# Optimization experiments

Measured on AMD Instinct MI355X. Metric: run time of the kernel, lower is better.

Reference implementation:

```python
import jax, jax.numpy as jnp
import numpy as np

F_BINS, T_STEPS, N_ACTIONS = 257, 65536, 256  # STFT bins, frames, codebook size


def setup_inputs() -> dict:
    key = jax.random.key(0)
    k1, k2, k3, k4 = jax.random.split(key, 4)
    x_out = jax.random.normal(k1, (F_BINS, T_STEPS), dtype=jnp.float32)
    x_source = jax.random.normal(k2, (F_BINS, T_STEPS), dtype=jnp.float32)
    x_clean = jax.random.normal(k3, (F_BINS, T_STEPS), dtype=jnp.float32)
    # G is self.G_mat = G_mat.T, i.e. [freq, action]; gains in [0,1)
    G = jax.random.uniform(k4, (F_BINS, N_ACTIONS), dtype=jnp.float32)
    return {"x_out": x_out, "x_source": x_source, "x_clean": x_clean, "G": G}


def reference(x_out, x_source, x_clean, G):
    # sums[t, a] = sum_f (x_clean[f, t] - G[f, a] * x_source[f, t])
    #            = sum_f x_clean[:, t]  -  (x_source^T @ G)[t, a]
    clean_sum = jnp.sum(x_clean, axis=0)                 # [T]
    proj = jnp.einsum('ft,fa->ta', x_source, G)          # [T, A]
    sums = clean_sum[:, None] - proj                     # [T, A]
    A_t = jnp.argmin(sums, axis=1)                       # [T], values in [0, A)
    F, T = x_source.shape
    # Faithful to the original loop: wiener_true[:, a] = G[:, a] for each
    # SELECTED ACTION a (column indexed by action id, not timestep).
    # Duplicate indices write identical values, so scatter-set is well-defined.
    wiener_true = jnp.zeros((F, T), dtype=x_source.dtype).at[:, A_t].set(G[:, A_t])
    true_out = (wiener_true * x_source).T                # [T, F]
    loss = jnp.mean((true_out - x_out.T) ** 2)
    return loss
```

## Files before the change

kernel.cpp:

```cpp
#include <hip/hip_runtime.h>

#define F_BINS  257
#define T_STEPS 65536
#define N_ACT   256
#define TM      256
#define NBLK_G  256
#define NTHR    512
#define XO_N4   4210688
#define XO_BLKS 514
#define PREP_BLKS 36

typedef float f32x4 __attribute__((ext_vector_type(4)));
typedef short s16x8 __attribute__((ext_vector_type(8)));
typedef unsigned u32x4 __attribute__((ext_vector_type(4)));

#define WS_PART  1024
#define WS_CORR  20480
#define WS_MASK  24576
#define WS_GFRAG 65536

__device__ __forceinline__ unsigned short f2bf_rne(float x) {
  unsigned u = __builtin_bit_cast(unsigned, x);
  return (unsigned short)((u + 0x7FFFu + ((u >> 16) & 1u)) >> 16);
}
__device__ __forceinline__ unsigned pack_bf(float hi, float lo) {
  return __builtin_amdgcn_perm(__builtin_bit_cast(unsigned, hi),
                               __builtin_bit_cast(unsigned, lo), 0x07060302u);
}

__global__ __launch_bounds__(256) void k_pre(
    const float* __restrict__ G, const float4* __restrict__ xo4,
    unsigned char* __restrict__ gfrag, double* __restrict__ partial) {
  const int tid = threadIdx.x;
  if (blockIdx.x < PREP_BLKS) {
    const int u = blockIdx.x * 256 + tid;
    const int lane = u & 63, ng = (u >> 6) & 15, kk = u >> 10;
    const int r16 = lane & 15, g = lane >> 4;
    const int a = ng * 16 + r16;
    unsigned short h[8];
#pragma unroll
    for (int j = 0; j < 8; ++j) {
      const int f = kk * 32 + 8 * g + j;
      h[j] = (f < F_BINS) ? f2bf_rne(G[f * N_ACT + a]) : (unsigned short)0;
    }
    u32x4 w;
#pragma unroll
    for (int i = 0; i < 4; ++i)
      w[i] = (unsigned)h[2 * i] | ((unsigned)h[2 * i + 1] << 16);
    *(u32x4*)(gfrag + (size_t)u * 16) = w;
    return;
  }
  const int b = blockIdx.x - PREP_BLKS;
  const size_t base = (size_t)b * 8192 + tid;
  double ds = 0.0;
#pragma unroll
  for (int r = 0; r < 2; ++r) {
    float4 v[16];
#pragma unroll
    for (int j = 0; j < 16; ++j) v[j] = xo4[base + (size_t)(r * 16 + j) * 256];
    float fs = 0.f;
#pragma unroll
    for (int j = 0; j < 16; ++j) {
      fs = fmaf(v[j].x, v[j].x, fs); fs = fmaf(v[j].y, v[j].y, fs);
      fs = fmaf(v[j].z, v[j].z, fs); fs = fmaf(v[j].w, v[j].w, fs);
    }
    ds += (double)fs;
  }
#pragma unroll
  for (int off = 32; off; off >>= 1) ds += __shfl_down(ds, off);
  __shared__ double sd[4];
  if ((tid & 63) == 0) sd[tid >> 6] = ds;
  __syncthreads();
  if (tid == 0) partial[b] = sd[0] + sd[1] + sd[2] + sd[3];
}

__global__ __launch_bounds__(NTHR, 2) void k_gemm(
    const float* __restrict__ xs, const unsigned char* __restrict__ gfrag,
    unsigned* __restrict__ maskp) {
  const int tid = threadIdx.x, lane = tid & 63, wv = tid >> 6;
  const int g = lane >> 4, r16 = lane & 15;
  const int t0 = blockIdx.x * TM;
  const int tcol = t0 + 32 * wv + 2 * r16;

  __shared__ __align__(16) unsigned char Bb[147456];
  __shared__ unsigned lmask[8];
  if (tid < 8) lmask[tid] = 0u;

#define LOADB(slot, kkv)                                                      \
  {                                                                           \
    _Pragma("unroll") for (int j = 0; j < 8; ++j) {                           \
      int f = 32 * (kkv) + 8 * g + j;                                         \
      if ((kkv) == 8) f = f > 256 ? 256 : f;   \
      va[slot][j] = *(const float2*)(xs + (size_t)f * T_STEPS + tcol);        \
    }                                                                         \
  }

  float2 va[4][8];
  LOADB(0, 0) LOADB(1, 1) LOADB(2, 2) LOADB(3, 3)
  __builtin_amdgcn_sched_barrier(0);
#pragma unroll
  for (int i = 0; i < 18; ++i) {
    const int c = 18 * wv + i;
    const unsigned char* src = gfrag + (size_t)c * 1024 + (size_t)lane * 16;
    unsigned char* dst = &Bb[c * 1024];
    __builtin_amdgcn_global_load_lds(
        (const __attribute__((address_space(1))) unsigned*)src,
        (__attribute__((address_space(3))) unsigned*)dst, 16, 0, 0);
  }
  __builtin_amdgcn_sched_barrier(0);

  s16x8 af[9][2];
#pragma unroll
  for (int kk = 0; kk < 9; ++kk) {
    const int b = kk & 3;
    af[kk][0] = __builtin_bit_cast(s16x8, (u32x4){
        pack_bf(va[b][1].x, va[b][0].x), pack_bf(va[b][3].x, va[b][2].x),
        pack_bf(va[b][5].x, va[b][4].x), pack_bf(va[b][7].x, va[b][6].x)});
    af[kk][1] = __builtin_bit_cast(s16x8, (u32x4){
        pack_bf(va[b][1].y, va[b][0].y), pack_bf(va[b][3].y, va[b][2].y),
        pack_bf(va[b][5].y, va[b][4].y), pack_bf(va[b][7].y, va[b][6].y)});
    if (kk + 4 <= 8) LOADB(b, kk + 4)
  }
#undef LOADB

  asm volatile("s_waitcnt vmcnt(0)" ::: "memory");
  __builtin_amdgcn_s_barrier();

  float bv[2][4]; int bc[2][4];
#pragma unroll
  for (int h = 0; h < 2; ++h) {
    f32x4 acc[2][8];
#pragma unroll
    for (int tau = 0; tau < 2; ++tau)
#pragma unroll
      for (int n = 0; n < 8; ++n) acc[tau][n] = (f32x4){0.f, 0.f, 0.f, 0.f};
#pragma unroll
    for (int kk = 0; kk < 9; ++kk) {
      const unsigned char* bp = &Bb[((kk * 16 + 8 * h) * 64 + lane) * 16];
#pragma unroll
      for (int n = 0; n < 8; ++n) {
        const s16x8 bfr = *(const s16x8*)(bp + n * 1024);
        acc[0][n] = __builtin_amdgcn_mfma_f32_16x16x32_bf16(
            af[kk][0], bfr, acc[0][n], 0, 0, 0);
        acc[1][n] = __builtin_amdgcn_mfma_f32_16x16x32_bf16(
            af[kk][1], bfr, acc[1][n], 0, 0, 0);
      }
    }
#pragma unroll
    for (int n = 0; n < 8; ++n) {
      const int c = 128 * h + 16 * n + r16;
#pragma unroll
      for (int tau = 0; tau < 2; ++tau)
#pragma unroll
        for (int q = 0; q < 4; ++q) {
          const float v = acc[tau][n][q];
          if (h == 0 && n == 0) { bv[tau][q] = v; bc[tau][q] = c; }
          else if (v > bv[tau][q]) { bv[tau][q] = v; bc[tau][q] = c; }
        }
    }
  }

#pragma unroll
  for (int m = 1; m <= 8; m <<= 1) {
#pragma unroll
    for (int tau = 0; tau < 2; ++tau)
#pragma unroll
      for (int q = 0; q < 4; ++q) {
        const float ov = __shfl_xor(bv[tau][q], m);
        const int   oc = __shfl_xor(bc[tau][q], m);
        if (ov > bv[tau][q] || (ov == bv[tau][q] && oc < bc[tau][q])) {
          bv[tau][q] = ov; bc[tau][q] = oc;
        }
      }
  }
  if (r16 == 0) {
#pragma unroll
    for (int tau = 0; tau < 2; ++tau)
#pragma unroll
      for (int q = 0; q < 4; ++q)
        atomicOr(&lmask[bc[tau][q] >> 5], 1u << (bc[tau][q] & 31));
  }
  __syncthreads();
  if (tid < 8) maskp[blockIdx.x * 8 + tid] = lmask[tid];
}

__global__ __launch_bounds__(256) void k_corr(
    const float* __restrict__ xs, const float* __restrict__ xo,
    const float* __restrict__ G, const unsigned* __restrict__ maskp,
    double* __restrict__ corrp) {
  __shared__ unsigned m8[8];
  const int tid = threadIdx.x;
  if (tid < 8) m8[tid] = 0u;
  __syncthreads();
  unsigned m = 0;
  for (int b = tid >> 3; b < NBLK_G; b += 32) m |= maskp[b * 8 + (tid & 7)];
  atomicOr(&m8[tid & 7], m);
  __syncthreads();
  const int f = blockIdx.x, a = tid;
  const bool sel = (m8[a >> 5] >> (a & 31)) & 1u;
  const float gv  = G[f * N_ACT + a];
  const float xsv = xs[(size_t)f * T_STEPS + a];
  const float xov = xo[(size_t)f * T_STEPS + a];
  const float gx  = gv * xsv;
  double acc = sel ? (double)(gx * (gx - 2.f * xov)) : 0.0;
#pragma unroll
  for (int off = 32; off; off >>= 1) acc += __shfl_down(acc, off);
  __shared__ double sdc[4];
  if ((tid & 63) == 0) sdc[tid >> 6] = acc;
  __syncthreads();
  if (tid == 0) corrp[f] = sdc[0] + sdc[1] + sdc[2] + sdc[3];
}

__global__ __launch_bounds__(256) void k_final(const double* __restrict__ partial,
                                               const double* __restrict__ corrp,
                                               float* __restrict__ out) {
  const int tid = threadIdx.x;
  double s = partial[tid] + partial[tid + 256] + corrp[tid];
  if (tid < 2) s += partial[tid + 512];
  if (tid == 0) s += corrp[256];
#pragma unroll
  for (int off = 32; off; off >>= 1) s += __shfl_down(s, off);
  __shared__ double sd[4];
  if ((tid & 63) == 0) sd[tid >> 6] = s;
  __syncthreads();
  if (tid == 0)
    out[0] = (float)((sd[0] + sd[1] + sd[2] + sd[3]) /
                     ((double)F_BINS * (double)T_STEPS));
}

extern "C" void kernel_launch(void* const* d_in, const int* in_sizes, int n_in,
                              void* d_out, int out_size, void* d_ws, size_t ws_size,
                              hipStream_t stream) {
  const float* x_out    = (const float*)d_in[0];
  const float* x_source = (const float*)d_in[1];
  const float* G        = (const float*)d_in[3];

  char* ws = (char*)d_ws;
  double*        partial = (double*)(ws + WS_PART);
  double*        corrp   = (double*)(ws + WS_CORR);
  unsigned*      maskp   = (unsigned*)(ws + WS_MASK);
  unsigned char* gfrag   = (unsigned char*)(ws + WS_GFRAG);

  k_pre  <<<PREP_BLKS + XO_BLKS, 256, 0, stream>>>(G, (const float4*)x_out,
                                                   gfrag, partial);
  k_gemm <<<NBLK_G, NTHR, 0, stream>>>(x_source, gfrag, maskp);
  k_corr <<<F_BINS, 256, 0, stream>>>(x_source, x_out, G, maskp, corrp);
  k_final<<<1, 256, 0, stream>>>(partial, corrp, (float*)d_out);
}
```

Before: 44.68 us.

## Fuse x_out sum-of-squares reduction into the GEMM kernel epilogue

Moves the x_out squared-sum reduction out of the preprocessing kernel and into the tail of the GEMM/argmin kernel. Each GEMM block reads its slice of x_out, prefetching the first chunk before the shuffle argmin reduction and double-buffering the rest. This removes a separate memory-bound pass that ran before the GEMM and overlaps the x_out traffic with GEMM work. In exchange it adds register pressure to a 512-thread, 2-blocks-per-CU kernel and lengthens its tail. The final reduction now reads one partial per GEMM block.

```diff
diff --git a/kernel.cpp b/kernel.cpp
--- a/kernel.cpp
+++ b/kernel.cpp
@@ -6,9 +6,8 @@
 #define TM      256
 #define NBLK_G  256
 #define NTHR    512
-#define XO_N4   4210688
-#define XO_BLKS 514
-#define PREP_BLKS 36
+#define XO_PB   16384
+#define XO_MAIN (NBLK_G * XO_PB)
 
 typedef float f32x4 __attribute__((ext_vector_type(4)));
 typedef short s16x8 __attribute__((ext_vector_type(8)));
@@ -28,55 +27,29 @@
                                __builtin_bit_cast(unsigned, lo), 0x07060302u);
 }
 
-__global__ __launch_bounds__(256) void k_pre(
-    const float* __restrict__ G, const float4* __restrict__ xo4,
-    unsigned char* __restrict__ gfrag, double* __restrict__ partial) {
-  const int tid = threadIdx.x;
-  if (blockIdx.x < PREP_BLKS) {
-    const int u = blockIdx.x * 256 + tid;
-    const int lane = u & 63, ng = (u >> 6) & 15, kk = u >> 10;
-    const int r16 = lane & 15, g = lane >> 4;
-    const int a = ng * 16 + r16;
-    unsigned short h[8];
-#pragma unroll
-    for (int j = 0; j < 8; ++j) {
-      const int f = kk * 32 + 8 * g + j;
-      h[j] = (f < F_BINS) ? f2bf_rne(G[f * N_ACT + a]) : (unsigned short)0;
-    }
-    u32x4 w;
-#pragma unroll
-    for (int i = 0; i < 4; ++i)
-      w[i] = (unsigned)h[2 * i] | ((unsigned)h[2 * i + 1] << 16);
-    *(u32x4*)(gfrag + (size_t)u * 16) = w;
-    return;
-  }
-  const int b = blockIdx.x - PREP_BLKS;
-  const size_t base = (size_t)b * 8192 + tid;
-  double ds = 0.0;
-#pragma unroll
-  for (int r = 0; r < 2; ++r) {
-    float4 v[16];
-#pragma unroll
-    for (int j = 0; j < 16; ++j) v[j] = xo4[base + (size_t)(r * 16 + j) * 256];
-    float fs = 0.f;
-#pragma unroll
-    for (int j = 0; j < 16; ++j) {
-      fs = fmaf(v[j].x, v[j].x, fs); fs = fmaf(v[j].y, v[j].y, fs);
-      fs = fmaf(v[j].z, v[j].z, fs); fs = fmaf(v[j].w, v[j].w, fs);
-    }
-    ds += (double)fs;
-  }
-#pragma unroll
-  for (int off = 32; off; off >>= 1) ds += __shfl_down(ds, off);
-  __shared__ double sd[4];
-  if ((tid & 63) == 0) sd[tid >> 6] = ds;
-  __syncthreads();
-  if (tid == 0) partial[b] = sd[0] + sd[1] + sd[2] + sd[3];
+__global__ __launch_bounds__(256) void k_prep(const float* __restrict__ G,
+                                              unsigned char* __restrict__ gfrag) {
+  const int u = blockIdx.x * 256 + threadIdx.x;
+  const int lane = u & 63, ng = (u >> 6) & 15, kk = u >> 10;
+  const int r16 = lane & 15, g = lane >> 4;
+  const int a = ng * 16 + r16;
+  unsigned short h[8];
+#pragma unroll
+  for (int j = 0; j < 8; ++j) {
+    const int f = kk * 32 + 8 * g + j;
+    h[j] = (f < F_BINS) ? f2bf_rne(G[f * N_ACT + a]) : (unsigned short)0;
+  }
+  u32x4 w;
+#pragma unroll
+  for (int i = 0; i < 4; ++i)
+    w[i] = (unsigned)h[2 * i] | ((unsigned)h[2 * i + 1] << 16);
+  *(u32x4*)(gfrag + (size_t)u * 16) = w;
 }
 
 __global__ __launch_bounds__(NTHR, 2) void k_gemm(
-    const float* __restrict__ xs, const unsigned char* __restrict__ gfrag,
-    unsigned* __restrict__ maskp) {
+    const float* __restrict__ xs, const float4* __restrict__ xo4,
+    const unsigned char* __restrict__ gfrag,
+    unsigned* __restrict__ maskp, double* __restrict__ partial) {
   const int tid = threadIdx.x, lane = tid & 63, wv = tid >> 6;
   const int g = lane >> 4, r16 = lane & 15;
   const int t0 = blockIdx.x * TM;
@@ -84,6 +57,7 @@
 
   __shared__ __align__(16) unsigned char Bb[147456];
   __shared__ unsigned lmask[8];
+  __shared__ double sdw[8];
   if (tid < 8) lmask[tid] = 0u;
 
 #define LOADB(slot, kkv)                                                      \
@@ -160,6 +134,13 @@
     }
   }
 
+  const float4* xop = xo4 + (size_t)blockIdx.x * XO_PB + tid;
+  float4 xv[2][8];
+#pragma unroll
+  for (int j = 0; j < 8; ++j) xv[0][j] = xop[j * 512];
+  float4 wrem = (float4){0.f, 0.f, 0.f, 0.f};
+  if (tid < 64) wrem = xo4[XO_MAIN + (size_t)blockIdx.x * 64 + tid];
+
 #pragma unroll
   for (int m = 1; m <= 8; m <<= 1) {
 #pragma unroll
@@ -182,6 +163,40 @@
   }
   __syncthreads();
   if (tid < 8) maskp[blockIdx.x * 8 + tid] = lmask[tid];
+
+  double ds = 0.0;
+#pragma unroll
+  for (int r = 0; r < 4; ++r) {
+    if (r + 1 < 4) {
+#pragma unroll
+      for (int j = 0; j < 8; ++j)
+        xv[(r + 1) & 1][j] = xop[(size_t)(r + 1) * 4096 + j * 512];
+    }
+    const float4* xc = xv[r & 1];
+    float fs = 0.f;
+#pragma unroll
+    for (int j = 0; j < 8; ++j) {
+      fs = fmaf(xc[j].x, xc[j].x, fs); fs = fmaf(xc[j].y, xc[j].y, fs);
+      fs = fmaf(xc[j].z, xc[j].z, fs); fs = fmaf(xc[j].w, xc[j].w, fs);
+    }
+    ds += (double)fs;
+  }
+  {
+    float fs = 0.f;
+    fs = fmaf(wrem.x, wrem.x, fs); fs = fmaf(wrem.y, wrem.y, fs);
+    fs = fmaf(wrem.z, wrem.z, fs); fs = fmaf(wrem.w, wrem.w, fs);
+    ds += (double)fs;
+  }
+#pragma unroll
+  for (int off = 32; off; off >>= 1) ds += __shfl_down(ds, off);
+  if (lane == 0) sdw[wv] = ds;
+  __syncthreads();
+  if (tid == 0) {
+    double s = 0.0;
+#pragma unroll
+    for (int w = 0; w < 8; ++w) s += sdw[w];
+    partial[blockIdx.x] = s;
+  }
 }
 
 __global__ __launch_bounds__(256) void k_corr(
@@ -215,8 +230,7 @@
                                                const double* __restrict__ corrp,
                                                float* __restrict__ out) {
   const int tid = threadIdx.x;
-  double s = partial[tid] + partial[tid + 256] + corrp[tid];
-  if (tid < 2) s += partial[tid + 512];
+  double s = partial[tid] + corrp[tid];
   if (tid == 0) s += corrp[256];
 #pragma unroll
   for (int off = 32; off; off >>= 1) s += __shfl_down(s, off);
@@ -241,9 +255,9 @@
   unsigned*      maskp   = (unsigned*)(ws + WS_MASK);
   unsigned char* gfrag   = (unsigned char*)(ws + WS_GFRAG);
 
-  k_pre  <<<PREP_BLKS + XO_BLKS, 256, 0, stream>>>(G, (const float4*)x_out,
-                                                   gfrag, partial);
-  k_gemm <<<NBLK_G, NTHR, 0, stream>>>(x_source, gfrag, maskp);
+  k_prep <<<36, 256, 0, stream>>>(G, gfrag);
+  k_gemm <<<NBLK_G, NTHR, 0, stream>>>(x_source, (const float4*)x_out,
+                                       gfrag, maskp, partial);
   k_corr <<<F_BINS, 256, 0, stream>>>(x_source, x_out, G, maskp, corrp);
   k_final<<<1, 256, 0, stream>>>(partial, corrp, (float*)d_out);
 }
```

New measurement: 46.65 us. 4.4% more time.

## Halve GEMM tile and stage G fragments per half to fit two blocks per CU

Applied to the files above, without the earlier changes.

The GEMM kernel now uses 4 waves per block over 128 timesteps, with twice as many blocks. Instead of holding all of G's bf16 fragments in LDS (about 144KB), each block stages only the half needed for the current action half (about 72KB) and reloads the second half between the two passes, with barriers around it. The aim is to let two blocks share a CU so one block's loads overlap the other's MFMA work. In exchange, the total G traffic from L2 doubles and each block gains an extra barrier-serialized stage between its halves.

```diff
diff --git a/kernel.cpp b/kernel.cpp
--- a/kernel.cpp
+++ b/kernel.cpp
@@ -3,9 +3,9 @@
 #define F_BINS  257
 #define T_STEPS 65536
 #define N_ACT   256
-#define TM      256
-#define NBLK_G  256
-#define NTHR    512
+#define TM      128
+#define NBLK_G  512
+#define NTHR    256
 #define XO_N4   4210688
 #define XO_BLKS 514
 #define PREP_BLKS 36
@@ -82,10 +82,23 @@
   const int t0 = blockIdx.x * TM;
   const int tcol = t0 + 32 * wv + 2 * r16;
 
-  __shared__ __align__(16) unsigned char Bb[147456];
+  __shared__ __align__(16) unsigned char Bh[73728];
   __shared__ unsigned lmask[8];
   if (tid < 8) lmask[tid] = 0u;
 
+#define STAGE_BH(hv)                                                          \
+  {                                                                           \
+    _Pragma("unroll") for (int idx = 0; idx < 18; ++idx) {                    \
+      const int j = 18 * wv + idx;                      \
+      const int kkc = j >> 3, ic = j & 7;                                     \
+      const unsigned char* src = gfrag +                                      \
+          (size_t)(kkc * 16 + 8 * (hv) + ic) * 1024 + (size_t)lane * 16;      \
+      unsigned char* dst = &Bh[j * 1024];                                     \
+      __builtin_amdgcn_global_load_lds(                                       \
+          (const __attribute__((address_space(1))) unsigned*)src,             \
+          (__attribute__((address_space(3))) unsigned*)dst, 16, 0, 0);        \
+    }                                                                         \
+  }
 #define LOADB(slot, kkv)                                                      \
   {                                                                           \
     _Pragma("unroll") for (int j = 0; j < 8; ++j) {                           \
@@ -98,15 +111,7 @@
   float2 va[4][8];
   LOADB(0, 0) LOADB(1, 1) LOADB(2, 2) LOADB(3, 3)
   __builtin_amdgcn_sched_barrier(0);
-#pragma unroll
-  for (int i = 0; i < 18; ++i) {
-    const int c = 18 * wv + i;
-    const unsigned char* src = gfrag + (size_t)c * 1024 + (size_t)lane * 16;
-    unsigned char* dst = &Bb[c * 1024];
-    __builtin_amdgcn_global_load_lds(
-        (const __attribute__((address_space(1))) unsigned*)src,
-        (__attribute__((address_space(3))) unsigned*)dst, 16, 0, 0);
-  }
+  STAGE_BH(0)
   __builtin_amdgcn_sched_barrier(0);
 
   s16x8 af[9][2];
@@ -123,12 +128,16 @@
   }
 #undef LOADB
 
-  asm volatile("s_waitcnt vmcnt(0)" ::: "memory");
-  __builtin_amdgcn_s_barrier();
+  __syncthreads();
 
   float bv[2][4]; int bc[2][4];
 #pragma unroll
   for (int h = 0; h < 2; ++h) {
+    if (h == 1) {
+      __syncthreads();
+      STAGE_BH(1)
+      __syncthreads();
+    }
     f32x4 acc[2][8];
 #pragma unroll
     for (int tau = 0; tau < 2; ++tau)
@@ -136,7 +145,7 @@
       for (int n = 0; n < 8; ++n) acc[tau][n] = (f32x4){0.f, 0.f, 0.f, 0.f};
 #pragma unroll
     for (int kk = 0; kk < 9; ++kk) {
-      const unsigned char* bp = &Bb[((kk * 16 + 8 * h) * 64 + lane) * 16];
+      const unsigned char* bp = &Bh[(kk * 8 * 64 + lane) * 16];
 #pragma unroll
       for (int n = 0; n < 8; ++n) {
         const s16x8 bfr = *(const s16x8*)(bp + n * 1024);
@@ -159,6 +168,7 @@
         }
     }
   }
+#undef STAGE_BH
 
 #pragma unroll
   for (int m = 1; m <= 8; m <<= 1) {
```

After: 43.52 us. 2.6% less time.
